# Performance work log

Hardware: AMD Instinct MI355X
Metric: run time of the kernel (lower is better)

## Reference

```python
import jax, jax.numpy as jnp
import numpy as np

N = 100000   # nodes per ntype (A and B)
E = 500000   # edges per canonical etype
D = 64       # embed_size


def setup_inputs() -> dict:
    key = jax.random.key(0)
    ks = jax.random.split(key, 16)
    inp = {}
    for i in range(4):
        inp[f"embed{i}"] = jax.random.normal(ks[i], (N, D), dtype=jnp.float32)
    inp["h_bias"] = jax.random.normal(ks[4], (D,), dtype=jnp.float32)
    for i in range(4):
        inp[f"src{i}"] = jax.random.randint(ks[5 + 2 * i], (E,), 0, N, dtype=jnp.int64)
        inp[f"dst{i}"] = jax.random.randint(ks[6 + 2 * i], (E,), 0, N, dtype=jnp.int64)
    return inp


def reference(embed0, embed1, embed2, embed3, h_bias,
              src0, dst0, src1, dst1, src2, dst2, src3, dst3):
    seg = jax.ops.segment_sum
    # canonical etypes: (A,r0,B), (B,r1,A), (A,r2,A), (B,r3,B)
    # multi_update_all with 'sum' cross-reducer: per dst ntype, sum of
    # scatter-added source embeddings over all incoming relations.
    h_A = seg(embed1[src1], dst1, num_segments=N) + seg(embed2[src2], dst2, num_segments=N)
    h_B = seg(embed0[src0], dst0, num_segments=N) + seg(embed3[src3], dst3, num_segments=N)
    # bias + activation (dropout p=0.0 is identity)
    h_A = jax.nn.relu(h_A + h_bias)
    h_B = jax.nn.relu(h_B + h_bias)
    return jnp.stack([h_A, h_B])  # [n_ntypes, N, D]
```

## Files before the change

kernel.cpp:

```cpp
#include <hip/hip_runtime.h>

#define NN 100000
#define EE 500000
#define DD 64
#define ND (NN * DD)
#define NSEG (2 * NN)
#define NEDGE (4 * EE)

#define BNODES 128
#define NBUCKET ((NSEG + BNODES - 1) / BNODES)
#define BCAP 1600

#define CB 1024
#define CT 8
#define EPB (CB * CT)
#define BPR ((EE + EPB - 1) / EPB)

__device__ __forceinline__ int rel_plane(int r) { return (r == 1 || r == 2) ? 0 : 1; }

#define WS_CURSOR 0
#define WS_ELIST  (NBUCKET)
#define WS_INTS   (NBUCKET + NBUCKET * BCAP)

__global__ void zero_cursor_kernel(int* __restrict__ cursor) {
    int i = blockIdx.x * blockDim.x + threadIdx.x;
    if (i < NBUCKET) cursor[i] = 0;
}

__global__ void bucket_fill_kernel(const int* __restrict__ src0,
                                   const int* __restrict__ dst0,
                                   const int* __restrict__ src1,
                                   const int* __restrict__ dst1,
                                   const int* __restrict__ src2,
                                   const int* __restrict__ dst2,
                                   const int* __restrict__ src3,
                                   const int* __restrict__ dst3,
                                   int* __restrict__ cursor,
                                   int* __restrict__ elist) {
    __shared__ int hist[NBUCKET];
    __shared__ int bpos[NBUCKET];
    int tid = threadIdx.x;
    for (int i = tid; i < NBUCKET; i += CB) hist[i] = 0;
    __syncthreads();

    int rel = blockIdx.x / BPR;
    int blk = blockIdx.x - rel * BPR;
    const int* src;
    const int* dst;
    if (rel == 0)      { src = src0; dst = dst0; }
    else if (rel == 1) { src = src1; dst = dst1; }
    else if (rel == 2) { src = src2; dst = dst2; }
    else               { src = src3; dst = dst3; }
    int plane = rel_plane(rel);
    int base = blk * EPB + tid * CT;

    int sv[CT], dv[CT];
    int nv;
    if (base + CT <= EE) {
        nv = CT;
        int4 a = *(const int4*)(src + base);
        int4 b = *(const int4*)(src + base + 4);
        sv[0] = a.x; sv[1] = a.y; sv[2] = a.z; sv[3] = a.w;
        sv[4] = b.x; sv[5] = b.y; sv[6] = b.z; sv[7] = b.w;
        int4 c = *(const int4*)(dst + base);
        int4 d = *(const int4*)(dst + base + 4);
        dv[0] = c.x; dv[1] = c.y; dv[2] = c.z; dv[3] = c.w;
        dv[4] = d.x; dv[5] = d.y; dv[6] = d.z; dv[7] = d.w;
    } else {
        nv = 0;
#pragma unroll
        for (int k = 0; k < CT; k++) {
            int e = base + k;
            if (e < EE) { sv[k] = src[e]; dv[k] = dst[e]; nv = k + 1; }
            else        { sv[k] = 0;      dv[k] = 0; }
        }
    }

#pragma unroll
    for (int k = 0; k < CT; k++) {
        if (k < nv) {
            int g = plane * NN + dv[k];
            atomicAdd(&hist[g >> 7], 1);
        }
    }
    __syncthreads();
    for (int i = tid; i < NBUCKET; i += CB) {
        int c = hist[i];
        bpos[i] = c ? atomicAdd(&cursor[i], c) : 0;
    }
    __syncthreads();
#pragma unroll
    for (int k = 0; k < CT; k++) {
        if (k < nv) {
            int g = plane * NN + dv[k];
            int b = g >> 7;
            int local = g & (BNODES - 1);
            int w = atomicAdd(&bpos[b], 1);
            if (w < BCAP) elist[b * BCAP + w] = sv[k] | (rel << 17) | (local << 19);
        }
    }
}

#define AB 1024
__global__ void accumulate_kernel(const float* __restrict__ e0,
                                  const float* __restrict__ e1,
                                  const float* __restrict__ e2,
                                  const float* __restrict__ e3,
                                  const float* __restrict__ bias,
                                  const int* __restrict__ cursor,
                                  const int* __restrict__ elist,
                                  float* __restrict__ out) {
    __shared__ int pl_lds[BCAP];
    __shared__ int sorted[BCAP];
    __shared__ int hcnt[BNODES];
    __shared__ int iscan[BNODES];
    __shared__ int rcur[BNODES];
    __shared__ float sbias[DD];

    int tid = threadIdx.x;
    int b = blockIdx.x;
    int cnt = cursor[b];
    if (cnt > BCAP) cnt = BCAP;

    if (tid < BNODES) hcnt[tid] = 0;
    if (tid < DD) sbias[tid] = bias[tid];
    __syncthreads();

    for (int j = tid; j < cnt; j += AB) {
        int p = elist[b * BCAP + j];
        pl_lds[j] = p;
        atomicAdd(&hcnt[(p >> 19) & (BNODES - 1)], 1);
    }
    __syncthreads();

    if (tid < BNODES) iscan[tid] = hcnt[tid];
    __syncthreads();
    for (int off = 1; off < BNODES; off <<= 1) {
        int v = 0;
        if (tid < BNODES && tid >= off) v = iscan[tid - off];
        __syncthreads();
        if (tid < BNODES) iscan[tid] += v;
        __syncthreads();
    }
    if (tid < BNODES) rcur[tid] = iscan[tid] - hcnt[tid];
    __syncthreads();

    for (int j = tid; j < cnt; j += AB) {
        int p = pl_lds[j];
        int pos = atomicAdd(&rcur[(p >> 19) & (BNODES - 1)], 1);
        sorted[pos] = p;
    }
    __syncthreads();

    int wave = tid >> 6;
    int lane = tid & 63;
    for (int ln = wave; ln < BNODES; ln += 16) {
        int seg = b * BNODES + ln;
        if (seg >= NSEG) break;
        int s1 = iscan[ln];
        int s0 = s1 - hcnt[ln];
        float acc = sbias[lane];
        int j = s0;
        for (; j + 4 <= s1; j += 4) {
            int p0 = sorted[j];
            int p1 = sorted[j + 1];
            int p2 = sorted[j + 2];
            int p3 = sorted[j + 3];
            int r0 = (p0 >> 17) & 3, s_0 = p0 & 0x1FFFF;
            int r1_ = (p1 >> 17) & 3, s_1 = p1 & 0x1FFFF;
            int r2_ = (p2 >> 17) & 3, s_2 = p2 & 0x1FFFF;
            int r3_ = (p3 >> 17) & 3, s_3 = p3 & 0x1FFFF;
            const float* t0 = (r0 == 0) ? e0 : (r0 == 1) ? e1 : (r0 == 2) ? e2 : e3;
            const float* t1 = (r1_ == 0) ? e0 : (r1_ == 1) ? e1 : (r1_ == 2) ? e2 : e3;
            const float* t2 = (r2_ == 0) ? e0 : (r2_ == 1) ? e1 : (r2_ == 2) ? e2 : e3;
            const float* t3 = (r3_ == 0) ? e0 : (r3_ == 1) ? e1 : (r3_ == 2) ? e2 : e3;
            float v0 = t0[(size_t)s_0 * DD + lane];
            float v1 = t1[(size_t)s_1 * DD + lane];
            float v2 = t2[(size_t)s_2 * DD + lane];
            float v3 = t3[(size_t)s_3 * DD + lane];
            acc += v0 + v1 + v2 + v3;
        }
        for (; j < s1; j++) {
            int p = sorted[j];
            int r = (p >> 17) & 3, s = p & 0x1FFFF;
            const float* t = (r == 0) ? e0 : (r == 1) ? e1 : (r == 2) ? e2 : e3;
            acc += t[(size_t)s * DD + lane];
        }
        out[(size_t)seg * DD + lane] = fmaxf(acc, 0.0f);
    }
}

__global__ void init_bias_kernel(float4* __restrict__ out,
                                 const float4* __restrict__ bias4,
                                 int n4) {
    int i = blockIdx.x * blockDim.x + threadIdx.x;
    if (i < n4) out[i] = bias4[i & 15];
}

__global__ void scatter_kernel(const float4* __restrict__ e0,
                               const float4* __restrict__ e1,
                               const float4* __restrict__ e2,
                               const float4* __restrict__ e3,
                               const int* __restrict__ src0,
                               const int* __restrict__ dst0,
                               const int* __restrict__ src1,
                               const int* __restrict__ dst1,
                               const int* __restrict__ src2,
                               const int* __restrict__ dst2,
                               const int* __restrict__ src3,
                               const int* __restrict__ dst3,
                               float* __restrict__ out) {
    long long t = (long long)blockIdx.x * blockDim.x + threadIdx.x;
    long long ge = t >> 4;
    int lane = (int)(t & 15);
    if (ge >= 4LL * EE) return;
    int rel = (int)(ge / EE);
    int e   = (int)(ge - (long long)rel * EE);
    const float4* emb; const int* src; const int* dst; float* outp;
    if (rel == 0)      { emb = e1; src = src1; dst = dst1; outp = out; }
    else if (rel == 1) { emb = e2; src = src2; dst = dst2; outp = out; }
    else if (rel == 2) { emb = e0; src = src0; dst = dst0; outp = out + ND; }
    else               { emb = e3; src = src3; dst = dst3; outp = out + ND; }
    int s = src[e]; int d = dst[e];
    float4 v = emb[(size_t)s * 16 + lane];
    float* o = outp + (size_t)d * 64 + lane * 4;
    unsafeAtomicAdd(o + 0, v.x);
    unsafeAtomicAdd(o + 1, v.y);
    unsafeAtomicAdd(o + 2, v.z);
    unsafeAtomicAdd(o + 3, v.w);
}

__global__ void relu_kernel(float4* __restrict__ out, int n4) {
    int i = blockIdx.x * blockDim.x + threadIdx.x;
    if (i < n4) {
        float4 v = out[i];
        v.x = fmaxf(v.x, 0.0f); v.y = fmaxf(v.y, 0.0f);
        v.z = fmaxf(v.z, 0.0f); v.w = fmaxf(v.w, 0.0f);
        out[i] = v;
    }
}

extern "C" void kernel_launch(void* const* d_in, const int* in_sizes, int n_in,
                              void* d_out, int out_size, void* d_ws, size_t ws_size,
                              hipStream_t stream) {
    const float* e0 = (const float*)d_in[0];
    const float* e1 = (const float*)d_in[1];
    const float* e2 = (const float*)d_in[2];
    const float* e3 = (const float*)d_in[3];
    const float* bias = (const float*)d_in[4];
    const int* src0 = (const int*)d_in[5];
    const int* dst0 = (const int*)d_in[6];
    const int* src1 = (const int*)d_in[7];
    const int* dst1 = (const int*)d_in[8];
    const int* src2 = (const int*)d_in[9];
    const int* dst2 = (const int*)d_in[10];
    const int* src3 = (const int*)d_in[11];
    const int* dst3 = (const int*)d_in[12];
    float* out = (float*)d_out;

    if (ws_size >= (size_t)WS_INTS * sizeof(int)) {
        int* ws = (int*)d_ws;
        int* cursor = ws + WS_CURSOR;
        int* elist  = ws + WS_ELIST;

        zero_cursor_kernel<<<(NBUCKET + 255) / 256, 256, 0, stream>>>(cursor);
        bucket_fill_kernel<<<4 * BPR, CB, 0, stream>>>(
            src0, dst0, src1, dst1, src2, dst2, src3, dst3, cursor, elist);
        accumulate_kernel<<<NBUCKET, AB, 0, stream>>>(
            e0, e1, e2, e3, bias, cursor, elist, out);
    } else {
        const int n4 = 2 * ND / 4;
        init_bias_kernel<<<(n4 + 255) / 256, 256, 0, stream>>>(
            (float4*)out, (const float4*)bias, n4);
        {
            long long threads = 4LL * EE * 16;
            long long grid = (threads + 255) / 256;
            scatter_kernel<<<(int)grid, 256, 0, stream>>>(
                (const float4*)e0, (const float4*)e1, (const float4*)e2, (const float4*)e3,
                src0, dst0, src1, dst1, src2, dst2, src3, dst3, out);
        }
        relu_kernel<<<(n4 + 255) / 256, 256, 0, stream>>>((float4*)out, n4);
    }
}
```

Baseline: 260.2 us.

## Widen buckets, reuse atomic ranks, and gather float4 rows four edges per wave

Buckets now cover 256 destination nodes with a larger capacity. In the fill and accumulate kernels, the rank returned by the first shared-memory atomic is kept in registers and reused, which removes the second atomic pass and the staging array. The accumulate loop now has each wave load float4 slices for four edges at once and reduce them with cross-lane shuffles. Bias and ReLU are applied once per node. The aim is fewer atomics and more gather loads in flight per wave, in exchange for more shared memory and registers per block and fewer blocks overall.

```diff
diff --git a/kernel.cpp b/kernel.cpp
--- a/kernel.cpp
+++ b/kernel.cpp
@@ -7,9 +7,9 @@
 #define NSEG (2 * NN)
 #define NEDGE (4 * EE)
 
-#define BNODES 128
+#define BNODES 256
 #define NBUCKET ((NSEG + BNODES - 1) / BNODES)
-#define BCAP 1600
+#define BCAP 3200
 
 #define CB 1024
 #define CT 8
@@ -17,6 +17,7 @@
 #define BPR ((EE + EPB - 1) / EPB)
 
 __device__ __forceinline__ int rel_plane(int r) { return (r == 1 || r == 2) ? 0 : 1; }
+
 
 #define WS_CURSOR 0
 #define WS_ELIST  (NBUCKET)
@@ -40,7 +41,7 @@
     __shared__ int hist[NBUCKET];
     __shared__ int bpos[NBUCKET];
     int tid = threadIdx.x;
-    for (int i = tid; i < NBUCKET; i += CB) hist[i] = 0;
+    if (tid < NBUCKET) hist[tid] = 0;
     __syncthreads();
 
     int rel = blockIdx.x / BPR;
@@ -76,11 +77,13 @@
         }
     }
 
+    int rank[CT], bkt[CT];
 #pragma unroll
     for (int k = 0; k < CT; k++) {
         if (k < nv) {
             int g = plane * NN + dv[k];
-            atomicAdd(&hist[g >> 7], 1);
+            bkt[k] = g >> 8;
+            rank[k] = atomicAdd(&hist[bkt[k]], 1);
         }
     }
     __syncthreads();
@@ -93,29 +96,26 @@
     for (int k = 0; k < CT; k++) {
         if (k < nv) {
             int g = plane * NN + dv[k];
-            int b = g >> 7;
-            int local = g & (BNODES - 1);
-            int w = atomicAdd(&bpos[b], 1);
-            if (w < BCAP) elist[b * BCAP + w] = sv[k] | (rel << 17) | (local << 19);
+            int w = bpos[bkt[k]] + rank[k];
+            if (w < BCAP)
+                elist[bkt[k] * BCAP + w] = sv[k] | (rel << 17) | ((g & 255) << 19);
         }
     }
 }
 
 #define AB 1024
+#define AITER 4
 __global__ void accumulate_kernel(const float* __restrict__ e0,
                                   const float* __restrict__ e1,
                                   const float* __restrict__ e2,
                                   const float* __restrict__ e3,
-                                  const float* __restrict__ bias,
+                                  const float4* __restrict__ bias4,
                                   const int* __restrict__ cursor,
                                   const int* __restrict__ elist,
-                                  float* __restrict__ out) {
-    __shared__ int pl_lds[BCAP];
+                                  float4* __restrict__ out4) {
     __shared__ int sorted[BCAP];
     __shared__ int hcnt[BNODES];
     __shared__ int iscan[BNODES];
-    __shared__ int rcur[BNODES];
-    __shared__ float sbias[DD];
 
     int tid = threadIdx.x;
     int b = blockIdx.x;
@@ -123,13 +123,15 @@
     if (cnt > BCAP) cnt = BCAP;
 
     if (tid < BNODES) hcnt[tid] = 0;
-    if (tid < DD) sbias[tid] = bias[tid];
-    __syncthreads();
-
+    __syncthreads();
+
+    int p_arr[AITER], r_arr[AITER];
+    int nk = 0;
     for (int j = tid; j < cnt; j += AB) {
         int p = elist[b * BCAP + j];
-        pl_lds[j] = p;
-        atomicAdd(&hcnt[(p >> 19) & (BNODES - 1)], 1);
+        p_arr[nk] = p;
+        r_arr[nk] = atomicAdd(&hcnt[(p >> 19) & (BNODES - 1)], 1);
+        nk++;
     }
     __syncthreads();
 
@@ -142,51 +144,52 @@
         if (tid < BNODES) iscan[tid] += v;
         __syncthreads();
     }
-    if (tid < BNODES) rcur[tid] = iscan[tid] - hcnt[tid];
-    __syncthreads();
-
-    for (int j = tid; j < cnt; j += AB) {
-        int p = pl_lds[j];
-        int pos = atomicAdd(&rcur[(p >> 19) & (BNODES - 1)], 1);
+
+    for (int k = 0; k < nk; k++) {
+        int p = p_arr[k];
+        int loc = (p >> 19) & (BNODES - 1);
+        int pos = iscan[loc] - hcnt[loc] + r_arr[k];
         sorted[pos] = p;
     }
     __syncthreads();
 
     int wave = tid >> 6;
     int lane = tid & 63;
+    int g = lane >> 4;
+    int q = lane & 15;
     for (int ln = wave; ln < BNODES; ln += 16) {
         int seg = b * BNODES + ln;
-        if (seg >= NSEG) break;
         int s1 = iscan[ln];
         int s0 = s1 - hcnt[ln];
-        float acc = sbias[lane];
-        int j = s0;
-        for (; j + 4 <= s1; j += 4) {
-            int p0 = sorted[j];
-            int p1 = sorted[j + 1];
-            int p2 = sorted[j + 2];
-            int p3 = sorted[j + 3];
-            int r0 = (p0 >> 17) & 3, s_0 = p0 & 0x1FFFF;
-            int r1_ = (p1 >> 17) & 3, s_1 = p1 & 0x1FFFF;
-            int r2_ = (p2 >> 17) & 3, s_2 = p2 & 0x1FFFF;
-            int r3_ = (p3 >> 17) & 3, s_3 = p3 & 0x1FFFF;
-            const float* t0 = (r0 == 0) ? e0 : (r0 == 1) ? e1 : (r0 == 2) ? e2 : e3;
-            const float* t1 = (r1_ == 0) ? e0 : (r1_ == 1) ? e1 : (r1_ == 2) ? e2 : e3;
-            const float* t2 = (r2_ == 0) ? e0 : (r2_ == 1) ? e1 : (r2_ == 2) ? e2 : e3;
-            const float* t3 = (r3_ == 0) ? e0 : (r3_ == 1) ? e1 : (r3_ == 2) ? e2 : e3;
-            float v0 = t0[(size_t)s_0 * DD + lane];
-            float v1 = t1[(size_t)s_1 * DD + lane];
-            float v2 = t2[(size_t)s_2 * DD + lane];
-            float v3 = t3[(size_t)s_3 * DD + lane];
-            acc += v0 + v1 + v2 + v3;
-        }
-        for (; j < s1; j++) {
-            int p = sorted[j];
-            int r = (p >> 17) & 3, s = p & 0x1FFFF;
+        float4 acc = make_float4(0.f, 0.f, 0.f, 0.f);
+        for (int j0 = s0; j0 < s1; j0 += 4) {
+            int j = j0 + g;
+            int jj = (j < s1) ? j : (s1 - 1);
+            int p = sorted[jj];
+            int s = p & 0x1FFFF;
+            int r = (p >> 17) & 3;
             const float* t = (r == 0) ? e0 : (r == 1) ? e1 : (r == 2) ? e2 : e3;
-            acc += t[(size_t)s * DD + lane];
-        }
-        out[(size_t)seg * DD + lane] = fmaxf(acc, 0.0f);
+            float4 v = *(const float4*)(t + (size_t)s * DD + q * 4);
+            if (j < s1) {
+                acc.x += v.x; acc.y += v.y; acc.z += v.z; acc.w += v.w;
+            }
+        }
+        acc.x += __shfl_xor(acc.x, 16, 64);
+        acc.y += __shfl_xor(acc.y, 16, 64);
+        acc.z += __shfl_xor(acc.z, 16, 64);
+        acc.w += __shfl_xor(acc.w, 16, 64);
+        acc.x += __shfl_xor(acc.x, 32, 64);
+        acc.y += __shfl_xor(acc.y, 32, 64);
+        acc.z += __shfl_xor(acc.z, 32, 64);
+        acc.w += __shfl_xor(acc.w, 32, 64);
+        float4 bb = bias4[q];
+        acc.x = fmaxf(acc.x + bb.x, 0.0f);
+        acc.y = fmaxf(acc.y + bb.y, 0.0f);
+        acc.z = fmaxf(acc.z + bb.z, 0.0f);
+        acc.w = fmaxf(acc.w + bb.w, 0.0f);
+        if (g == 0 && seg < NSEG) {
+            out4[(size_t)seg * 16 + q] = acc;
+        }
     }
 }
 
@@ -267,7 +270,7 @@
         bucket_fill_kernel<<<4 * BPR, CB, 0, stream>>>(
             src0, dst0, src1, dst1, src2, dst2, src3, dst3, cursor, elist);
         accumulate_kernel<<<NBUCKET, AB, 0, stream>>>(
-            e0, e1, e2, e3, bias, cursor, elist, out);
+            e0, e1, e2, e3, (const float4*)bias, cursor, elist, (float4*)out);
     } else {
         const int n4 = 2 * ND / 4;
         init_bias_kernel<<<(n4 + 255) / 256, 256, 0, stream>>>(
```

Result: faster. 253.2 us (-2.7%).
